# Kernel tuning notes

Hardware: AMD Instinct MI355X
Metric: run time of the kernel (lower is better)

The kernel has to match this reference:

```python
import jax, jax.numpy as jnp
import numpy as np

B, L, D, H = 2, 2048, 1024, 16
HD = D // H


def _xavier(key, out_f, in_f):
    std = (2.0 / (in_f + out_f)) ** 0.5
    return jax.random.normal(key, (out_f, in_f), dtype=jnp.float32) * std


def setup_inputs() -> dict:
    key = jax.random.key(0)
    k = jax.random.split(key, 8)
    Q = jax.random.normal(k[0], (B, L, D), dtype=jnp.float32)
    K = jax.random.normal(k[1], (B, L, D), dtype=jnp.float32)
    V = jax.random.normal(k[2], (B, L, D), dtype=jnp.float32)
    mask = jnp.tril(jnp.ones((L, L), dtype=jnp.int32))[None, None]  # causal [1,1,L,L]
    wq = _xavier(k[3], D, D)
    wk = _xavier(k[4], D, D)
    wv = _xavier(k[5], D, D)
    wo = _xavier(k[6], D, D)
    bo = jnp.zeros((D,), dtype=jnp.float32)
    return {"Q": Q, "K": K, "V": V, "mask": mask,
            "wq": wq, "wk": wk, "wv": wv, "wo": wo, "bo": bo}


def reference(Q, K, V, mask, wq, wk, wv, wo, bo):
    N, Lq, Dm = Q.shape
    # projections: X @ W^T (Linear stores [out, in])
    q = (Q @ wq.T).reshape(N, Lq, H, HD).transpose(0, 2, 1, 3)  # [N,H,L,hd]
    kk = (K @ wk.T).reshape(N, Lq, H, HD).transpose(0, 2, 1, 3)
    v = (V @ wv.T).reshape(N, Lq, H, HD).transpose(0, 2, 1, 3)
    score = jnp.einsum('bhqd,bhkd->bhqk', q, kk) / jnp.sqrt(jnp.float32(HD))
    score = jnp.where(mask == 0, -jnp.inf, score)
    weights = jax.nn.softmax(score, axis=-1)
    attn = jnp.einsum('bhqk,bhkd->bhqd', weights, v)
    out = attn.transpose(0, 2, 1, 3).reshape(N, Lq, Dm)
    return out @ wo.T + bo
```

## Files before the change

kernel.cpp:

```cpp
#include <hip/hip_runtime.h>
#include <hip/hip_bf16.h>


#define B_ 2
#define L_ 2048
#define D_ 1024
#define H_ 16
#define HD_ 64
#define NA_ ((size_t)B_ * L_ * D_)
#define NW_ ((size_t)D_ * D_)

typedef __attribute__((ext_vector_type(8))) short bf16x8;
typedef __attribute__((ext_vector_type(4))) float f32x4;
typedef __hip_bfloat16 bf16;

__device__ __forceinline__ void async_load16(const void* g, void* l) {
  __builtin_amdgcn_global_load_lds((const __attribute__((address_space(1))) void*)g,
                                   (__attribute__((address_space(3))) void*)l,
                                   16, 0, 0);
}

__global__ __launch_bounds__(256) void xcvt_kernel(const float* __restrict__ q,
                                                   const float* __restrict__ k,
                                                   const float* __restrict__ v,
                                                   const float* __restrict__ w0,
                                                   const float* __restrict__ w1,
                                                   const float* __restrict__ w2,
                                                   const float* __restrict__ w3,
                                                   bf16* __restrict__ dst) {
  const int y = blockIdx.y;
  const float* src = (y == 0) ? q : (y == 1) ? k : (y == 2) ? v
                   : (y == 3) ? w0 : (y == 4) ? w1 : (y == 5) ? w2 : w3;
  const size_t n = (y < 3) ? NA_ : NW_;
  const size_t off = (y < 3) ? (size_t)y * NA_ : 3 * NA_ + (size_t)(y - 3) * NW_;
  size_t i = ((size_t)blockIdx.x * 256 + threadIdx.x) * 4;
  if (i >= n) return;
  float4 vv = *(const float4*)(src + i);
  union { bf16 h[4]; uint2 u; } pk;
  pk.h[0] = __float2bfloat16(vv.x);
  pk.h[1] = __float2bfloat16(vv.y);
  pk.h[2] = __float2bfloat16(vv.z);
  pk.h[3] = __float2bfloat16(vv.w);
  *(uint2*)(dst + off + i) = pk.u;
}

__global__ __launch_bounds__(256) void gemm_qkv(const bf16* __restrict__ Qb,
                                                const bf16* __restrict__ Kb,
                                                const bf16* __restrict__ Vb,
                                                const bf16* __restrict__ Wb,
                                                bf16* __restrict__ qp,
                                                bf16* __restrict__ kp,
                                                bf16* __restrict__ vtp) {
  __shared__ __align__(16) bf16 As[128 * 32];
  __shared__ __align__(16) bf16 Bs[128 * 32];
  const int tid = threadIdx.x;
  const int wv = tid >> 6, lane = tid & 63;
  const int quad = lane >> 4, l16 = lane & 15;
  const int wm = wv & 1, wn = wv >> 1;
  const int m0 = blockIdx.x * 128, n0 = blockIdx.y * 128;
  const int z = blockIdx.z;
  const bf16* X = (z == 0) ? Qb : (z == 1) ? Kb : Vb;
  const bf16* W = Wb + (size_t)z * NW_;

  f32x4 acc[4][4];
#pragma unroll
  for (int i = 0; i < 4; i++)
#pragma unroll
    for (int j = 0; j < 4; j++) acc[i][j] = (f32x4){0.f, 0.f, 0.f, 0.f};

  for (int k0 = 0; k0 < D_; k0 += 32) {
#pragma unroll
    for (int it = 0; it < 2; it++) {
      int c = (wv * 2 + it) * 64 + lane;
      int row = c >> 2, cc = c & 3;
      async_load16(X + (size_t)(m0 + row) * D_ + k0 + cc * 8, (char*)As + c * 16);
      async_load16(W + (size_t)(n0 + row) * D_ + k0 + cc * 8, (char*)Bs + c * 16);
    }
    __syncthreads();
    bf16x8 af[4], bfr[4];
#pragma unroll
    for (int mi = 0; mi < 4; mi++)
      af[mi] = *(const bf16x8*)&As[(wm * 64 + mi * 16 + l16) * 32 + quad * 8];
#pragma unroll
    for (int ni = 0; ni < 4; ni++)
      bfr[ni] = *(const bf16x8*)&Bs[(wn * 64 + ni * 16 + l16) * 32 + quad * 8];
#pragma unroll
    for (int mi = 0; mi < 4; mi++)
#pragma unroll
      for (int ni = 0; ni < 4; ni++)
        acc[mi][ni] = __builtin_amdgcn_mfma_f32_16x16x32_bf16(af[mi], bfr[ni],
                                                              acc[mi][ni], 0, 0, 0);
    __syncthreads();
  }

  const float sc = (z == 0) ? 0.125f : 1.0f;
#pragma unroll
  for (int mi = 0; mi < 4; mi++) {
#pragma unroll
    for (int ni = 0; ni < 4; ni++) {
      int n = n0 + wn * 64 + ni * 16 + l16;
#pragma unroll
      for (int r = 0; r < 4; r++) {
        int m = m0 + wm * 64 + mi * 16 + quad * 4 + r;
        bf16 v = __float2bfloat16(acc[mi][ni][r] * sc);
        if (z == 2) {
          int b = m >> 11, l = m & (L_ - 1);
          int h = n >> 6, hd = n & 63;
          vtp[((size_t)((b * H_ + h) * HD_ + hd)) * L_ + l] = v;
        } else {
          ((z == 0) ? qp : kp)[(size_t)m * D_ + n] = v;
        }
      }
    }
  }
}

__global__ __launch_bounds__(256) void attn_kernel(const bf16* __restrict__ qp,
                                                   const bf16* __restrict__ kp,
                                                   const bf16* __restrict__ vt,
                                                   bf16* __restrict__ attn) {
  __shared__ __align__(16) bf16 Kt[2][64 * 64];
  __shared__ __align__(16) bf16 Vt[2][64 * 64];
  __shared__ __align__(16) bf16 Pl[4][16 * 72];
  __shared__ __align__(16) bf16 Ph[4][16 * 72];
  const int tid = threadIdx.x;
  const int wv = tid >> 6, lane = tid & 63;
  const int quad = lane >> 4, l16 = lane & 15;
  const int pair = blockIdx.x, h = blockIdx.y, b = blockIdx.z;
  const int qlo = pair, qhi = (L_ / 64 - 1) - pair;

  const int rL = qlo * 64 + wv * 16 + l16;
  const int rH = qhi * 64 + wv * 16 + l16;
  bf16x8 qaL[2], qaH[2];
#pragma unroll
  for (int kk = 0; kk < 2; kk++) {
    qaL[kk] = *(const bf16x8*)&qp[((size_t)(b * L_ + rL)) * D_ + h * HD_ +
                                  kk * 32 + quad * 8];
    qaH[kk] = *(const bf16x8*)&qp[((size_t)(b * L_ + rH)) * D_ + h * HD_ +
                                  kk * 32 + quad * 8];
  }

  f32x4 OL[4], OH[4];
#pragma unroll
  for (int t = 0; t < 4; t++) {
    OL[t] = (f32x4){0.f, 0.f, 0.f, 0.f};
    OH[t] = (f32x4){0.f, 0.f, 0.f, 0.f};
  }
  float lL[4] = {0.f, 0.f, 0.f, 0.f}, lH[4] = {0.f, 0.f, 0.f, 0.f};

  const int csw = quad ^ (l16 & 7);

  auto stage = [&](int j, int buf) {
    const int j0 = j * 64;
#pragma unroll
    for (int it = 0; it < 2; it++) {
      int slot = (wv * 2 + it) * 64 + lane;
      int row = slot >> 3, c = (slot & 7) ^ (row & 7);
      async_load16(kp + ((size_t)(b * L_ + j0 + row)) * D_ + h * HD_ + c * 8,
                   (char*)Kt[buf] + slot * 16);
      async_load16(vt + ((size_t)((b * H_ + h) * HD_ + row)) * L_ + j0 + c * 8,
                   (char*)Vt[buf] + slot * 16);
    }
  };

  stage(0, 0);
  for (int j = 0; j <= qhi; j++) {
    const int buf = j & 1;
    const int j0 = j * 64;
    const bool doLo = (j <= qlo);
    __syncthreads();
    if (j < qhi) stage(j + 1, buf ^ 1);

    f32x4 sL[4], sH[4];
#pragma unroll
    for (int ss = 0; ss < 4; ss++) {
      int krow = ss * 16 + l16;
      bf16x8 kb0 = *(const bf16x8*)&Kt[buf][krow * 64 + csw * 8];
      bf16x8 kb1 = *(const bf16x8*)&Kt[buf][krow * 64 + (csw ^ 4) * 8];
      f32x4 s = (f32x4){0.f, 0.f, 0.f, 0.f};
      s = __builtin_amdgcn_mfma_f32_16x16x32_bf16(qaH[0], kb0, s, 0, 0, 0);
      s = __builtin_amdgcn_mfma_f32_16x16x32_bf16(qaH[1], kb1, s, 0, 0, 0);
      sH[ss] = s;
      if (doLo) {
        f32x4 t = (f32x4){0.f, 0.f, 0.f, 0.f};
        t = __builtin_amdgcn_mfma_f32_16x16x32_bf16(qaL[0], kb0, t, 0, 0, 0);
        t = __builtin_amdgcn_mfma_f32_16x16x32_bf16(qaL[1], kb1, t, 0, 0, 0);
        sL[ss] = t;
      }
    }

    if (j == qhi) {
#pragma unroll
      for (int ss = 0; ss < 4; ss++) {
        int key = j0 + ss * 16 + l16;
#pragma unroll
        for (int r = 0; r < 4; r++) {
          int rq = qhi * 64 + wv * 16 + quad * 4 + r;
          if (key > rq) sH[ss][r] = -1e30f;
        }
      }
    }
    if (doLo && j == qlo) {
#pragma unroll
      for (int ss = 0; ss < 4; ss++) {
        int key = j0 + ss * 16 + l16;
#pragma unroll
        for (int r = 0; r < 4; r++) {
          int rq = qlo * 64 + wv * 16 + quad * 4 + r;
          if (key > rq) sL[ss][r] = -1e30f;
        }
      }
    }
#pragma unroll
    for (int ss = 0; ss < 4; ss++) {
#pragma unroll
      for (int r = 0; r < 4; r++) {
        float p = __expf(sH[ss][r]);
        lH[r] += p;
        Ph[wv][(quad * 4 + r) * 72 + ss * 16 + l16] = __float2bfloat16(p);
      }
    }
    if (doLo) {
#pragma unroll
      for (int ss = 0; ss < 4; ss++) {
#pragma unroll
        for (int r = 0; r < 4; r++) {
          float p = __expf(sL[ss][r]);
          lL[r] += p;
          Pl[wv][(quad * 4 + r) * 72 + ss * 16 + l16] = __float2bfloat16(p);
        }
      }
    }

    asm volatile("s_waitcnt lgkmcnt(0)" ::: "memory");

#pragma unroll
    for (int kk = 0; kk < 2; kk++) {
      bf16x8 pah = *(const bf16x8*)&Ph[wv][l16 * 72 + kk * 32 + quad * 8];
      bf16x8 pal;
      if (doLo) pal = *(const bf16x8*)&Pl[wv][l16 * 72 + kk * 32 + quad * 8];
#pragma unroll
      for (int t = 0; t < 4; t++) {
        bf16x8 vb = *(const bf16x8*)&Vt[buf][(t * 16 + l16) * 64 + (csw ^ (kk * 4)) * 8];
        OH[t] = __builtin_amdgcn_mfma_f32_16x16x32_bf16(pah, vb, OH[t], 0, 0, 0);
        if (doLo) OL[t] = __builtin_amdgcn_mfma_f32_16x16x32_bf16(pal, vb, OL[t], 0, 0, 0);
      }
    }
  }

#pragma unroll
  for (int r = 0; r < 4; r++) {
#pragma unroll
    for (int off = 1; off < 16; off <<= 1) {
      lL[r] += __shfl_xor(lL[r], off, 64);
      lH[r] += __shfl_xor(lH[r], off, 64);
    }
  }
#pragma unroll
  for (int t = 0; t < 4; t++) {
#pragma unroll
    for (int r = 0; r < 4; r++) {
      int rowL = qlo * 64 + wv * 16 + quad * 4 + r;
      int rowH = qhi * 64 + wv * 16 + quad * 4 + r;
      attn[((size_t)(b * L_ + rowL)) * D_ + h * HD_ + t * 16 + l16] =
          __float2bfloat16(OL[t][r] / lL[r]);
      attn[((size_t)(b * L_ + rowH)) * D_ + h * HD_ + t * 16 + l16] =
          __float2bfloat16(OH[t][r] / lH[r]);
    }
  }
}

__global__ __launch_bounds__(256) void gemm_out(const bf16* __restrict__ X,
                                                const bf16* __restrict__ W,
                                                const float* __restrict__ bias,
                                                float* __restrict__ out) {
  __shared__ __align__(16) bf16 As[64 * 32];
  __shared__ __align__(16) bf16 Bs[128 * 32];
  const int tid = threadIdx.x;
  const int wv = tid >> 6, lane = tid & 63;
  const int quad = lane >> 4, l16 = lane & 15;
  const int wm = wv & 1, wn = wv >> 1;
  const int m0 = blockIdx.x * 64, n0 = blockIdx.y * 128;

  f32x4 acc[2][4];
#pragma unroll
  for (int i = 0; i < 2; i++)
#pragma unroll
    for (int j = 0; j < 4; j++) acc[i][j] = (f32x4){0.f, 0.f, 0.f, 0.f};

  for (int k0 = 0; k0 < D_; k0 += 32) {
    {
      int c = tid;
      int row = c >> 2, cc = c & 3;
      async_load16(X + (size_t)(m0 + row) * D_ + k0 + cc * 8, (char*)As + c * 16);
    }
#pragma unroll
    for (int it = 0; it < 2; it++) {
      int c = (wv * 2 + it) * 64 + lane;
      int row = c >> 2, cc = c & 3;
      async_load16(W + (size_t)(n0 + row) * D_ + k0 + cc * 8, (char*)Bs + c * 16);
    }
    __syncthreads();
    bf16x8 af[2], bfr[4];
#pragma unroll
    for (int mi = 0; mi < 2; mi++)
      af[mi] = *(const bf16x8*)&As[(wm * 32 + mi * 16 + l16) * 32 + quad * 8];
#pragma unroll
    for (int ni = 0; ni < 4; ni++)
      bfr[ni] = *(const bf16x8*)&Bs[(wn * 64 + ni * 16 + l16) * 32 + quad * 8];
#pragma unroll
    for (int mi = 0; mi < 2; mi++)
#pragma unroll
      for (int ni = 0; ni < 4; ni++)
        acc[mi][ni] = __builtin_amdgcn_mfma_f32_16x16x32_bf16(af[mi], bfr[ni],
                                                              acc[mi][ni], 0, 0, 0);
    __syncthreads();
  }

#pragma unroll
  for (int mi = 0; mi < 2; mi++) {
#pragma unroll
    for (int ni = 0; ni < 4; ni++) {
      int n = n0 + wn * 64 + ni * 16 + l16;
      float bval = bias[n];
#pragma unroll
      for (int r = 0; r < 4; r++) {
        int m = m0 + wm * 32 + mi * 16 + quad * 4 + r;
        out[(size_t)m * D_ + n] = acc[mi][ni][r] + bval;
      }
    }
  }
}

extern "C" void kernel_launch(void* const* d_in, const int* in_sizes, int n_in,
                              void* d_out, int out_size, void* d_ws, size_t ws_size,
                              hipStream_t stream) {
  const float* Q  = (const float*)d_in[0];
  const float* K  = (const float*)d_in[1];
  const float* V  = (const float*)d_in[2];
  const float* wq = (const float*)d_in[4];
  const float* wk = (const float*)d_in[5];
  const float* wvp = (const float*)d_in[6];
  const float* wo = (const float*)d_in[7];
  const float* bo = (const float*)d_in[8];
  float* out = (float*)d_out;

  bf16* base = (bf16*)d_ws;
  bf16* Qb = base;
  bf16* Kb = Qb + NA_;
  bf16* Vb = Kb + NA_;
  bf16* Wb = Vb + NA_;
  bf16* qp = Wb + 4 * NW_;
  bf16* kp = qp + NA_;
  bf16* vt = kp + NA_;
  bf16* at = vt + NA_;

  xcvt_kernel<<<dim3(NA_ / 1024, 7), 256, 0, stream>>>(Q, K, V, wq, wk, wvp, wo, base);
  gemm_qkv<<<dim3(32, 8, 3), 256, 0, stream>>>(Qb, Kb, Vb, Wb, qp, kp, vt);
  attn_kernel<<<dim3(L_ / 128, H_, B_), 256, 0, stream>>>(qp, kp, vt, at);
  gemm_out<<<dim3(64, 8), 256, 0, stream>>>(at, Wb + 3 * NW_, bo, out);
}
```

Measured before the change: 238.9 us.

## Double GEMM K-tile to 64 with XOR-swizzled LDS and exp2 softmax

Both projection GEMMs now stage a 64-wide K slice per iteration instead of 32. This halves the number of barrier pairs and load rounds. LDS columns are XOR-swizzled by row to avoid bank conflicts on the wider rows. The Q scale folds in log2(e) so attention can use exp2f instead of __expf, which removes a multiply per exponential. LDS use per block doubles, which may reduce occupancy.

```diff
diff --git a/kernel.cpp b/kernel.cpp
--- a/kernel.cpp
+++ b/kernel.cpp
@@ -51,8 +51,8 @@
                                                 bf16* __restrict__ qp,
                                                 bf16* __restrict__ kp,
                                                 bf16* __restrict__ vtp) {
-  __shared__ __align__(16) bf16 As[128 * 32];
-  __shared__ __align__(16) bf16 Bs[128 * 32];
+  __shared__ __align__(16) bf16 As[128 * 64];
+  __shared__ __align__(16) bf16 Bs[128 * 64];
   const int tid = threadIdx.x;
   const int wv = tid >> 6, lane = tid & 63;
   const int quad = lane >> 4, l16 = lane & 15;
@@ -61,6 +61,7 @@
   const int z = blockIdx.z;
   const bf16* X = (z == 0) ? Qb : (z == 1) ? Kb : Vb;
   const bf16* W = Wb + (size_t)z * NW_;
+  const int sw = l16 & 7;
 
   f32x4 acc[4][4];
 #pragma unroll
@@ -68,32 +69,36 @@
 #pragma unroll
     for (int j = 0; j < 4; j++) acc[i][j] = (f32x4){0.f, 0.f, 0.f, 0.f};
 
-  for (int k0 = 0; k0 < D_; k0 += 32) {
-#pragma unroll
-    for (int it = 0; it < 2; it++) {
-      int c = (wv * 2 + it) * 64 + lane;
-      int row = c >> 2, cc = c & 3;
-      async_load16(X + (size_t)(m0 + row) * D_ + k0 + cc * 8, (char*)As + c * 16);
-      async_load16(W + (size_t)(n0 + row) * D_ + k0 + cc * 8, (char*)Bs + c * 16);
-    }
-    __syncthreads();
-    bf16x8 af[4], bfr[4];
-#pragma unroll
-    for (int mi = 0; mi < 4; mi++)
-      af[mi] = *(const bf16x8*)&As[(wm * 64 + mi * 16 + l16) * 32 + quad * 8];
-#pragma unroll
-    for (int ni = 0; ni < 4; ni++)
-      bfr[ni] = *(const bf16x8*)&Bs[(wn * 64 + ni * 16 + l16) * 32 + quad * 8];
-#pragma unroll
-    for (int mi = 0; mi < 4; mi++)
+  for (int k0 = 0; k0 < D_; k0 += 64) {
+#pragma unroll
+    for (int it = 0; it < 4; it++) {
+      int s = it * 256 + tid;
+      int row = s >> 3, c = (s & 7) ^ (row & 7);
+      async_load16(X + (size_t)(m0 + row) * D_ + k0 + c * 8, (char*)As + s * 16);
+      async_load16(W + (size_t)(n0 + row) * D_ + k0 + c * 8, (char*)Bs + s * 16);
+    }
+    __syncthreads();
+#pragma unroll
+    for (int kk = 0; kk < 2; kk++) {
+      const int slot = ((kk << 2) | quad) ^ sw;
+      bf16x8 af[4], bfr[4];
+#pragma unroll
+      for (int mi = 0; mi < 4; mi++)
+        af[mi] = *(const bf16x8*)&As[(wm * 64 + mi * 16 + l16) * 64 + slot * 8];
 #pragma unroll
       for (int ni = 0; ni < 4; ni++)
-        acc[mi][ni] = __builtin_amdgcn_mfma_f32_16x16x32_bf16(af[mi], bfr[ni],
-                                                              acc[mi][ni], 0, 0, 0);
-    __syncthreads();
-  }
-
-  const float sc = (z == 0) ? 0.125f : 1.0f;
+        bfr[ni] = *(const bf16x8*)&Bs[(wn * 64 + ni * 16 + l16) * 64 + slot * 8];
+#pragma unroll
+      for (int mi = 0; mi < 4; mi++)
+#pragma unroll
+        for (int ni = 0; ni < 4; ni++)
+          acc[mi][ni] = __builtin_amdgcn_mfma_f32_16x16x32_bf16(af[mi], bfr[ni],
+                                                                acc[mi][ni], 0, 0, 0);
+    }
+    __syncthreads();
+  }
+
+  const float sc = (z == 0) ? 0.125f * 1.44269504f : 1.0f;
 #pragma unroll
   for (int mi = 0; mi < 4; mi++) {
 #pragma unroll
@@ -215,7 +220,7 @@
     for (int ss = 0; ss < 4; ss++) {
 #pragma unroll
       for (int r = 0; r < 4; r++) {
-        float p = __expf(sH[ss][r]);
+        float p = exp2f(sH[ss][r]);
         lH[r] += p;
         Ph[wv][(quad * 4 + r) * 72 + ss * 16 + l16] = __float2bfloat16(p);
       }
@@ -225,7 +230,7 @@
       for (int ss = 0; ss < 4; ss++) {
 #pragma unroll
         for (int r = 0; r < 4; r++) {
-          float p = __expf(sL[ss][r]);
+          float p = exp2f(sL[ss][r]);
           lL[r] += p;
           Pl[wv][(quad * 4 + r) * 72 + ss * 16 + l16] = __float2bfloat16(p);
         }
@@ -274,13 +279,14 @@
                                                 const bf16* __restrict__ W,
                                                 const float* __restrict__ bias,
                                                 float* __restrict__ out) {
-  __shared__ __align__(16) bf16 As[64 * 32];
-  __shared__ __align__(16) bf16 Bs[128 * 32];
+  __shared__ __align__(16) bf16 As[64 * 64];
+  __shared__ __align__(16) bf16 Bs[128 * 64];
   const int tid = threadIdx.x;
   const int wv = tid >> 6, lane = tid & 63;
   const int quad = lane >> 4, l16 = lane & 15;
   const int wm = wv & 1, wn = wv >> 1;
   const int m0 = blockIdx.x * 64, n0 = blockIdx.y * 128;
+  const int sw = l16 & 7;
 
   f32x4 acc[2][4];
 #pragma unroll
@@ -288,32 +294,37 @@
 #pragma unroll
     for (int j = 0; j < 4; j++) acc[i][j] = (f32x4){0.f, 0.f, 0.f, 0.f};
 
-  for (int k0 = 0; k0 < D_; k0 += 32) {
-    {
-      int c = tid;
-      int row = c >> 2, cc = c & 3;
-      async_load16(X + (size_t)(m0 + row) * D_ + k0 + cc * 8, (char*)As + c * 16);
-    }
+  for (int k0 = 0; k0 < D_; k0 += 64) {
 #pragma unroll
     for (int it = 0; it < 2; it++) {
-      int c = (wv * 2 + it) * 64 + lane;
-      int row = c >> 2, cc = c & 3;
-      async_load16(W + (size_t)(n0 + row) * D_ + k0 + cc * 8, (char*)Bs + c * 16);
-    }
-    __syncthreads();
-    bf16x8 af[2], bfr[4];
-#pragma unroll
-    for (int mi = 0; mi < 2; mi++)
-      af[mi] = *(const bf16x8*)&As[(wm * 32 + mi * 16 + l16) * 32 + quad * 8];
-#pragma unroll
-    for (int ni = 0; ni < 4; ni++)
-      bfr[ni] = *(const bf16x8*)&Bs[(wn * 64 + ni * 16 + l16) * 32 + quad * 8];
-#pragma unroll
-    for (int mi = 0; mi < 2; mi++)
+      int s = it * 256 + tid;
+      int row = s >> 3, c = (s & 7) ^ (row & 7);
+      async_load16(X + (size_t)(m0 + row) * D_ + k0 + c * 8, (char*)As + s * 16);
+    }
+#pragma unroll
+    for (int it = 0; it < 4; it++) {
+      int s = it * 256 + tid;
+      int row = s >> 3, c = (s & 7) ^ (row & 7);
+      async_load16(W + (size_t)(n0 + row) * D_ + k0 + c * 8, (char*)Bs + s * 16);
+    }
+    __syncthreads();
+#pragma unroll
+    for (int kk = 0; kk < 2; kk++) {
+      const int slot = ((kk << 2) | quad) ^ sw;
+      bf16x8 af[2], bfr[4];
+#pragma unroll
+      for (int mi = 0; mi < 2; mi++)
+        af[mi] = *(const bf16x8*)&As[(wm * 32 + mi * 16 + l16) * 64 + slot * 8];
 #pragma unroll
       for (int ni = 0; ni < 4; ni++)
-        acc[mi][ni] = __builtin_amdgcn_mfma_f32_16x16x32_bf16(af[mi], bfr[ni],
-                                                              acc[mi][ni], 0, 0, 0);
+        bfr[ni] = *(const bf16x8*)&Bs[(wn * 64 + ni * 16 + l16) * 64 + slot * 8];
+#pragma unroll
+      for (int mi = 0; mi < 2; mi++)
+#pragma unroll
+        for (int ni = 0; ni < 4; ni++)
+          acc[mi][ni] = __builtin_amdgcn_mfma_f32_16x16x32_bf16(af[mi], bfr[ni],
+                                                                acc[mi][ni], 0, 0, 0);
+    }
     __syncthreads();
   }
 
```

After: 251.5 us. 5.3% more time.
